# Kernel tuning notes

Hardware: AMD Instinct MI355X
Metric: run time of the kernel (lower is better)

The kernel has to match this reference:

```python
import jax, jax.numpy as jnp
import numpy as np


def setup_inputs() -> dict:
    key = jax.random.key(0)
    ks = jax.random.split(key, 13)
    B, D, H, O = 4096, 2048, 3, 1  # batch, input_dim, hidden layer count, output_dim
    f32 = jnp.float32
    scale = 1.0 / np.sqrt(D)
    return {
        "x": jax.random.normal(ks[0], (B, D), f32),
        "w_mu_h": jax.random.normal(ks[1], (H, D, D), f32) * scale,
        "w_rho_h": jax.random.normal(ks[2], (H, D, D), f32) - 5.0,  # softplus(-5) ~ small std
        "b_mu_h": jax.random.normal(ks[3], (H, D), f32) * scale,
        "b_rho_h": jax.random.normal(ks[4], (H, D), f32) - 5.0,
        "w_mu_o": jax.random.normal(ks[5], (O, D), f32) * scale,
        "w_rho_o": jax.random.normal(ks[6], (O, D), f32) - 5.0,
        "b_mu_o": jax.random.normal(ks[7], (O,), f32) * scale,
        "b_rho_o": jax.random.normal(ks[8], (O,), f32) - 5.0,
        # reparameterization noise (torch.randn_like), passed explicitly for determinism
        "eps_w_h": jax.random.normal(ks[9], (H, D, D), f32),
        "eps_b_h": jax.random.normal(ks[10], (H, D), f32),
        "eps_w_o": jax.random.normal(ks[11], (O, D), f32),
        "eps_b_o": jax.random.normal(ks[12], (O,), f32),
    }


def _vlinear(x, w_mu, w_rho, b_mu, b_rho, eps_w, eps_b):
    # weight = mu + eps * softplus(rho); F.linear(x, W, b) = x @ W.T + b
    w = w_mu + eps_w * jax.nn.softplus(w_rho)
    b = b_mu + eps_b * jax.nn.softplus(b_rho)
    return x @ w.T + b


def reference(x, w_mu_h, w_rho_h, b_mu_h, b_rho_h,
              w_mu_o, w_rho_o, b_mu_o, b_rho_o,
              eps_w_h, eps_b_h, eps_w_o, eps_b_o):
    def step(h, p):
        wm, wr, bm, br, ew, eb = p
        h = jax.nn.relu(_vlinear(h, wm, wr, bm, br, ew, eb))
        return h, None

    h, _ = jax.lax.scan(step, x, (w_mu_h, w_rho_h, b_mu_h, b_rho_h, eps_w_h, eps_b_h))
    return _vlinear(h, w_mu_o, w_rho_o, b_mu_o, b_rho_o, eps_w_o, eps_b_o)
```

## Files before the change

kernel.cpp:

```cpp
#include <hip/hip_runtime.h>

#define BB 4096
#define DD 2048

typedef float f32x4 __attribute__((ext_vector_type(4)));
typedef __bf16 bf16x8 __attribute__((ext_vector_type(8)));

typedef __attribute__((address_space(1))) unsigned int gl_u32;
typedef __attribute__((address_space(3))) unsigned int lds_u32;

#define GLOAD_LDS16(gptr, sptr) \
  __builtin_amdgcn_global_load_lds((gl_u32*)(void*)(gptr), (lds_u32*)(sptr), 16, 0, 0)

__device__ __forceinline__ unsigned short f2bf(float f) {
  unsigned int u = __float_as_uint(f);
  u += 0x7fffu + ((u >> 16) & 1u);
  return (unsigned short)(u >> 16);
}

__device__ __forceinline__ float sp(float x) {
  float t = __expf(-fabsf(x));
  return fmaxf(x, 0.0f) + __logf(1.0f + t);
}

__device__ __forceinline__ void prep_w_vec4(
    const float* __restrict__ mu, const float* __restrict__ rho,
    const float* __restrict__ eps, unsigned short* __restrict__ Wh,
    long long i)
{
  float4 m = ((const float4*)mu)[i];
  float4 r = ((const float4*)rho)[i];
  float4 e = ((const float4*)eps)[i];
  ushort4 o;
  o.x = f2bf(m.x + e.x * sp(r.x));
  o.y = f2bf(m.y + e.y * sp(r.y));
  o.z = f2bf(m.z + e.z * sp(r.z));
  o.w = f2bf(m.w + e.w * sp(r.w));
  ((ushort4*)Wh)[i] = o;
}

__device__ __forceinline__ void prep_f32_vec4(
    const float* __restrict__ mu, const float* __restrict__ rho,
    const float* __restrict__ eps, float* __restrict__ out, long long i)
{
  float4 m = ((const float4*)mu)[i];
  float4 r = ((const float4*)rho)[i];
  float4 e = ((const float4*)eps)[i];
  float4 o;
  o.x = m.x + e.x * sp(r.x);
  o.y = m.y + e.y * sp(r.y);
  o.z = m.z + e.z * sp(r.z);
  o.w = m.w + e.w * sp(r.w);
  ((float4*)out)[i] = o;
}

__global__ __launch_bounds__(512) void prep0_kernel(
    const float* __restrict__ x,
    const float* __restrict__ wmuh, const float* __restrict__ wrhoh,
    const float* __restrict__ bmuh, const float* __restrict__ brhoh,
    const float* __restrict__ epswh, const float* __restrict__ epsbh,
    unsigned short* __restrict__ Wh, unsigned short* __restrict__ Xb,
    float* __restrict__ bh)
{
  const int b = blockIdx.x;
  const int t = threadIdx.x;
  if (b < 512) {
    long long base = (long long)b * 2048 + t;
    #pragma unroll
    for (int j = 0; j < 4; ++j)
      prep_w_vec4(wmuh, wrhoh, epswh, Wh, base + j * 512);
    return;
  }
  if (b < 1536) {
    long long base = (long long)(b - 512) * 2048 + t;
    #pragma unroll
    for (int j = 0; j < 4; ++j) {
      float4 v = ((const float4*)x)[base + j * 512];
      ushort4 o;
      o.x = f2bf(v.x); o.y = f2bf(v.y); o.z = f2bf(v.z); o.w = f2bf(v.w);
      ((ushort4*)Xb)[base + j * 512] = o;
    }
    return;
  }
  prep_f32_vec4(bmuh, brhoh, epsbh, bh, t);
}

#define NGEMM 512

__global__ __launch_bounds__(512, 4) void gemm_relu_fused_kernel(
    const unsigned short* __restrict__ A,
    const unsigned short* __restrict__ W,
    const float* __restrict__ bias,
    unsigned short* __restrict__ C,
    int N, int K, int fuse_prep,
    const float* __restrict__ wmuh, const float* __restrict__ wrhoh,
    const float* __restrict__ bmuh, const float* __restrict__ brhoh,
    const float* __restrict__ wmuo, const float* __restrict__ wrhoo,
    const float* __restrict__ bmuo, const float* __restrict__ brhoo,
    const float* __restrict__ epswh, const float* __restrict__ epsbh,
    const float* __restrict__ epswo, const float* __restrict__ epsbo,
    unsigned short* __restrict__ Wh, float* __restrict__ bh,
    float* __restrict__ wo, float* __restrict__ bo)
{
  __shared__ unsigned short sA[128 * 64];
  __shared__ unsigned short sB[128 * 64];

  const int id = blockIdx.x;
  const int t = threadIdx.x;

  if (id >= NGEMM) {
    const int pb = id - NGEMM;
    if (pb < 1024) {
      long long base = 1048576LL + (long long)pb * 2048 + t;
      #pragma unroll
      for (int j = 0; j < 4; ++j)
        prep_w_vec4(wmuh, wrhoh, epswh, Wh, base + j * 512);
      return;
    }
    #pragma unroll
    for (int j = 0; j < 2; ++j)
      prep_f32_vec4(bmuh, brhoh, epsbh, bh, 512 + j * 512 + t);
    prep_f32_vec4(wmuo, wrhoo, epswo, wo, t);
    if (t == 0) bo[0] = bmuo[0] + epsbo[0] * sp(brhoo[0]);
    return;
  }

  const int w = t >> 6;
  const int l = t & 63;
  const int lq = l >> 4;
  const int lr = l & 15;

  const int p = id & 7;
  const int i4 = id >> 3;
  const int mt = (p & 3) * 8 + (i4 & 7);
  const int nt = (p >> 2) * 8 + (i4 >> 3);
  const int m0 = mt * 128;
  const int n0 = nt * 128;

  const int mw = (w >> 2) * 64;
  const int nw = (w & 3) * 32;

  f32x4 acc[4][2] = {};

  int srow[2], sgc[2];
  #pragma unroll
  for (int i = 0; i < 2; ++i) {
    int c = i * 512 + t;
    srow[i] = c >> 3;
    sgc[i] = (c & 7) ^ (srow[i] & 7);
  }

  for (int kt = 0; kt < K; kt += 64) {
    #pragma unroll
    for (int i = 0; i < 2; ++i) {
      int c = i * 512 + t;
      const unsigned short* ga = A + (size_t)(m0 + srow[i]) * K + kt + sgc[i] * 8;
      GLOAD_LDS16(ga, &sA[c * 8]);
      const unsigned short* gb = W + (size_t)(n0 + srow[i]) * K + kt + sgc[i] * 8;
      GLOAD_LDS16(gb, &sB[c * 8]);
    }
    __syncthreads();

    #pragma unroll
    for (int s = 0; s < 2; ++s) {
      bf16x8 af[4], bfr[2];
      int g = s * 4 + lq;
      #pragma unroll
      for (int i = 0; i < 4; ++i) {
        int ra = mw + i * 16 + lr;
        af[i] = *(const bf16x8*)&sA[ra * 64 + (g ^ (ra & 7)) * 8];
      }
      #pragma unroll
      for (int j = 0; j < 2; ++j) {
        int rb = nw + j * 16 + lr;
        bfr[j] = *(const bf16x8*)&sB[rb * 64 + (g ^ (rb & 7)) * 8];
      }
      #pragma unroll
      for (int i = 0; i < 4; ++i)
        #pragma unroll
        for (int j = 0; j < 2; ++j)
          acc[i][j] = __builtin_amdgcn_mfma_f32_16x16x32_bf16(af[i], bfr[j], acc[i][j], 0, 0, 0);
    }
    __syncthreads();
  }

  #pragma unroll
  for (int j = 0; j < 2; ++j) {
    int n = n0 + nw + j * 16 + lr;
    float bv = bias[n];
    #pragma unroll
    for (int i = 0; i < 4; ++i) {
      int mbase = m0 + mw + i * 16 + lq * 4;
      #pragma unroll
      for (int r = 0; r < 4; ++r) {
        float v = acc[i][j][r] + bv;
        v = fmaxf(v, 0.0f);
        C[(size_t)(mbase + r) * N + n] = f2bf(v);
      }
    }
  }
}

__global__ __launch_bounds__(512, 4) void gemm_relu_kernel(
    const unsigned short* __restrict__ A,
    const unsigned short* __restrict__ W,
    const float* __restrict__ bias,
    unsigned short* __restrict__ C,
    int N, int K)
{
  __shared__ unsigned short sA[128 * 64];
  __shared__ unsigned short sB[128 * 64];

  const int t = threadIdx.x;
  const int w = t >> 6;
  const int l = t & 63;
  const int lq = l >> 4;
  const int lr = l & 15;

  const int id = blockIdx.x;
  const int p = id & 7;
  const int i4 = id >> 3;
  const int mt = (p & 3) * 8 + (i4 & 7);
  const int nt = (p >> 2) * 8 + (i4 >> 3);
  const int m0 = mt * 128;
  const int n0 = nt * 128;

  const int mw = (w >> 2) * 64;
  const int nw = (w & 3) * 32;

  f32x4 acc[4][2] = {};

  int srow[2], sgc[2];
  #pragma unroll
  for (int i = 0; i < 2; ++i) {
    int c = i * 512 + t;
    srow[i] = c >> 3;
    sgc[i] = (c & 7) ^ (srow[i] & 7);
  }

  for (int kt = 0; kt < K; kt += 64) {
    #pragma unroll
    for (int i = 0; i < 2; ++i) {
      int c = i * 512 + t;
      const unsigned short* ga = A + (size_t)(m0 + srow[i]) * K + kt + sgc[i] * 8;
      GLOAD_LDS16(ga, &sA[c * 8]);
      const unsigned short* gb = W + (size_t)(n0 + srow[i]) * K + kt + sgc[i] * 8;
      GLOAD_LDS16(gb, &sB[c * 8]);
    }
    __syncthreads();

    #pragma unroll
    for (int s = 0; s < 2; ++s) {
      bf16x8 af[4], bfr[2];
      int g = s * 4 + lq;
      #pragma unroll
      for (int i = 0; i < 4; ++i) {
        int ra = mw + i * 16 + lr;
        af[i] = *(const bf16x8*)&sA[ra * 64 + (g ^ (ra & 7)) * 8];
      }
      #pragma unroll
      for (int j = 0; j < 2; ++j) {
        int rb = nw + j * 16 + lr;
        bfr[j] = *(const bf16x8*)&sB[rb * 64 + (g ^ (rb & 7)) * 8];
      }
      #pragma unroll
      for (int i = 0; i < 4; ++i)
        #pragma unroll
        for (int j = 0; j < 2; ++j)
          acc[i][j] = __builtin_amdgcn_mfma_f32_16x16x32_bf16(af[i], bfr[j], acc[i][j], 0, 0, 0);
    }
    __syncthreads();
  }

  #pragma unroll
  for (int j = 0; j < 2; ++j) {
    int n = n0 + nw + j * 16 + lr;
    float bv = bias[n];
    #pragma unroll
    for (int i = 0; i < 4; ++i) {
      int mbase = m0 + mw + i * 16 + lq * 4;
      #pragma unroll
      for (int r = 0; r < 4; ++r) {
        float v = acc[i][j][r] + bv;
        v = fmaxf(v, 0.0f);
        C[(size_t)(mbase + r) * N + n] = f2bf(v);
      }
    }
  }
}

__global__ void final_kernel(const unsigned short* __restrict__ H,
                             const float* __restrict__ wo,
                             const float* __restrict__ bo,
                             float* __restrict__ out)
{
  const int row = blockIdx.x * 4 + (threadIdx.x >> 6);
  const int l = threadIdx.x & 63;
  const unsigned short* hr = H + (size_t)row * DD;
  float sum = 0.0f;
  #pragma unroll
  for (int s = 0; s < 4; ++s) {
    int k = s * 512 + l * 8;
    uint4 hv = *(const uint4*)&hr[k];
    float4 w0 = *(const float4*)&wo[k];
    float4 w1 = *(const float4*)&wo[k + 4];
    sum += __uint_as_float(hv.x << 16) * w0.x;
    sum += __uint_as_float(hv.x & 0xffff0000u) * w0.y;
    sum += __uint_as_float(hv.y << 16) * w0.z;
    sum += __uint_as_float(hv.y & 0xffff0000u) * w0.w;
    sum += __uint_as_float(hv.z << 16) * w1.x;
    sum += __uint_as_float(hv.z & 0xffff0000u) * w1.y;
    sum += __uint_as_float(hv.w << 16) * w1.z;
    sum += __uint_as_float(hv.w & 0xffff0000u) * w1.w;
  }
  #pragma unroll
  for (int off = 32; off > 0; off >>= 1)
    sum += __shfl_down(sum, off, 64);
  if (l == 0) out[row] = sum + bo[0];
}

extern "C" void kernel_launch(void* const* d_in, const int* in_sizes, int n_in,
                              void* d_out, int out_size, void* d_ws, size_t ws_size,
                              hipStream_t stream) {
  const float* x     = (const float*)d_in[0];
  const float* wmuh  = (const float*)d_in[1];
  const float* wrhoh = (const float*)d_in[2];
  const float* bmuh  = (const float*)d_in[3];
  const float* brhoh = (const float*)d_in[4];
  const float* wmuo  = (const float*)d_in[5];
  const float* wrhoo = (const float*)d_in[6];
  const float* bmuo  = (const float*)d_in[7];
  const float* brhoo = (const float*)d_in[8];
  const float* epswh = (const float*)d_in[9];
  const float* epsbh = (const float*)d_in[10];
  const float* epswo = (const float*)d_in[11];
  const float* epsbo = (const float*)d_in[12];

  char* ws = (char*)d_ws;
  unsigned short* Wh = (unsigned short*)(ws);
  unsigned short* Xb = (unsigned short*)(ws + 25165824);
  unsigned short* Ha = (unsigned short*)(ws + 25165824 + 16777216);
  unsigned short* Hb = (unsigned short*)(ws + 25165824 + 2 * 16777216);
  float* bh = (float*)(ws + 25165824 + 3 * 16777216);
  float* wo = (float*)(ws + 25165824 + 3 * 16777216 + 24576);
  float* bo = (float*)(ws + 25165824 + 3 * 16777216 + 24576 + 8192);

  prep0_kernel<<<1537, 512, 0, stream>>>(
      x, wmuh, wrhoh, bmuh, brhoh, epswh, epsbh, Wh, Xb, bh);

  gemm_relu_fused_kernel<<<NGEMM + 1025, 512, 0, stream>>>(
      Xb, Wh, bh, Ha, DD, DD, 1,
      wmuh, wrhoh, bmuh, brhoh, wmuo, wrhoo, bmuo, brhoo,
      epswh, epsbh, epswo, epsbo, Wh, bh, wo, bo);

  gemm_relu_kernel<<<NGEMM, 512, 0, stream>>>(Ha, Wh + 1 * 4194304, bh + DD,     Hb, DD, DD);
  gemm_relu_kernel<<<NGEMM, 512, 0, stream>>>(Hb, Wh + 2 * 4194304, bh + 2 * DD, Xb, DD, DD);

  final_kernel<<<BB / 4, 256, 0, stream>>>(Xb, wo, bo, (float*)d_out);
}
```

Before: 304.8 us.

## Fuse output-layer dot product into last hidden GEMM epilogue

The third hidden GEMM no longer writes its bf16 activation matrix. Its epilogue applies bias and ReLU, multiplies by the output weights, and reduces across lanes and waves into per-N-tile partial sums. A small kernel then adds the 16 partials and the output bias. This removes a 16MB store and reload plus the separate output-layer kernel, at the cost of shuffle and LDS reduction work in the epilogue and one extra launch. The shared GEMM code is also factored into inline helpers.

```diff
diff --git a/kernel.cpp b/kernel.cpp
--- a/kernel.cpp
+++ b/kernel.cpp
@@ -87,20 +87,109 @@
 
 #define NGEMM 512
 
+struct GemmCoords { int m0, n0, mw, nw; int srow[2], sgc[2]; };
+
+__device__ __forceinline__ GemmCoords gemm_coords(int id, int t) {
+  GemmCoords g;
+  const int w = t >> 6;
+  const int p = id & 7;
+  const int i4 = id >> 3;
+  const int mt = (p & 3) * 8 + (i4 & 7);
+  const int nt = (p >> 2) * 8 + (i4 >> 3);
+  g.m0 = mt * 128;
+  g.n0 = nt * 128;
+  g.mw = (w >> 2) * 64;
+  g.nw = (w & 3) * 32;
+  #pragma unroll
+  for (int i = 0; i < 2; ++i) {
+    int c = i * 512 + t;
+    g.srow[i] = c >> 3;
+    g.sgc[i] = (c & 7) ^ (g.srow[i] & 7);
+  }
+  return g;
+}
+
+__device__ __forceinline__ void gemm_mainloop(
+    const unsigned short* __restrict__ A,
+    const unsigned short* __restrict__ W,
+    unsigned short* sA, unsigned short* sB,
+    const GemmCoords& gc, int t, f32x4 (&acc)[4][2])
+{
+  const int K = DD;
+  const int l = t & 63;
+  const int lq = l >> 4;
+  const int lr = l & 15;
+  for (int kt = 0; kt < K; kt += 64) {
+    #pragma unroll
+    for (int i = 0; i < 2; ++i) {
+      int c = i * 512 + t;
+      const unsigned short* ga = A + (size_t)(gc.m0 + gc.srow[i]) * K + kt + gc.sgc[i] * 8;
+      GLOAD_LDS16(ga, &sA[c * 8]);
+      const unsigned short* gb = W + (size_t)(gc.n0 + gc.srow[i]) * K + kt + gc.sgc[i] * 8;
+      GLOAD_LDS16(gb, &sB[c * 8]);
+    }
+    __syncthreads();
+
+    #pragma unroll
+    for (int s = 0; s < 2; ++s) {
+      bf16x8 af[4], bfr[2];
+      int g = s * 4 + lq;
+      #pragma unroll
+      for (int i = 0; i < 4; ++i) {
+        int ra = gc.mw + i * 16 + lr;
+        af[i] = *(const bf16x8*)&sA[ra * 64 + (g ^ (ra & 7)) * 8];
+      }
+      #pragma unroll
+      for (int j = 0; j < 2; ++j) {
+        int rb = gc.nw + j * 16 + lr;
+        bfr[j] = *(const bf16x8*)&sB[rb * 64 + (g ^ (rb & 7)) * 8];
+      }
+      #pragma unroll
+      for (int i = 0; i < 4; ++i)
+        #pragma unroll
+        for (int j = 0; j < 2; ++j)
+          acc[i][j] = __builtin_amdgcn_mfma_f32_16x16x32_bf16(af[i], bfr[j], acc[i][j], 0, 0, 0);
+    }
+    __syncthreads();
+  }
+}
+
+__device__ __forceinline__ void gemm_epilogue_store(
+    const GemmCoords& gc, int t, f32x4 (&acc)[4][2],
+    const float* __restrict__ bias, unsigned short* __restrict__ C)
+{
+  const int N = DD;
+  const int l = t & 63;
+  const int lq = l >> 4;
+  const int lr = l & 15;
+  #pragma unroll
+  for (int j = 0; j < 2; ++j) {
+    int n = gc.n0 + gc.nw + j * 16 + lr;
+    float bv = bias[n];
+    #pragma unroll
+    for (int i = 0; i < 4; ++i) {
+      int mbase = gc.m0 + gc.mw + i * 16 + lq * 4;
+      #pragma unroll
+      for (int r = 0; r < 4; ++r) {
+        float v = fmaxf(acc[i][j][r] + bv, 0.0f);
+        C[(size_t)(mbase + r) * N + n] = f2bf(v);
+      }
+    }
+  }
+}
+
 __global__ __launch_bounds__(512, 4) void gemm_relu_fused_kernel(
     const unsigned short* __restrict__ A,
     const unsigned short* __restrict__ W,
     const float* __restrict__ bias,
     unsigned short* __restrict__ C,
-    int N, int K, int fuse_prep,
     const float* __restrict__ wmuh, const float* __restrict__ wrhoh,
     const float* __restrict__ bmuh, const float* __restrict__ brhoh,
     const float* __restrict__ wmuo, const float* __restrict__ wrhoo,
-    const float* __restrict__ bmuo, const float* __restrict__ brhoo,
     const float* __restrict__ epswh, const float* __restrict__ epsbh,
-    const float* __restrict__ epswo, const float* __restrict__ epsbo,
+    const float* __restrict__ epswo,
     unsigned short* __restrict__ Wh, float* __restrict__ bh,
-    float* __restrict__ wo, float* __restrict__ bo)
+    float* __restrict__ wo)
 {
   __shared__ unsigned short sA[128 * 64];
   __shared__ unsigned short sB[128 * 64];
@@ -121,202 +210,104 @@
     for (int j = 0; j < 2; ++j)
       prep_f32_vec4(bmuh, brhoh, epsbh, bh, 512 + j * 512 + t);
     prep_f32_vec4(wmuo, wrhoo, epswo, wo, t);
-    if (t == 0) bo[0] = bmuo[0] + epsbo[0] * sp(brhoo[0]);
     return;
   }
 
-  const int w = t >> 6;
-  const int l = t & 63;
-  const int lq = l >> 4;
-  const int lr = l & 15;
-
-  const int p = id & 7;
-  const int i4 = id >> 3;
-  const int mt = (p & 3) * 8 + (i4 & 7);
-  const int nt = (p >> 2) * 8 + (i4 >> 3);
-  const int m0 = mt * 128;
-  const int n0 = nt * 128;
-
-  const int mw = (w >> 2) * 64;
-  const int nw = (w & 3) * 32;
-
+  GemmCoords gc = gemm_coords(id, t);
   f32x4 acc[4][2] = {};
-
-  int srow[2], sgc[2];
-  #pragma unroll
-  for (int i = 0; i < 2; ++i) {
-    int c = i * 512 + t;
-    srow[i] = c >> 3;
-    sgc[i] = (c & 7) ^ (srow[i] & 7);
-  }
-
-  for (int kt = 0; kt < K; kt += 64) {
-    #pragma unroll
-    for (int i = 0; i < 2; ++i) {
-      int c = i * 512 + t;
-      const unsigned short* ga = A + (size_t)(m0 + srow[i]) * K + kt + sgc[i] * 8;
-      GLOAD_LDS16(ga, &sA[c * 8]);
-      const unsigned short* gb = W + (size_t)(n0 + srow[i]) * K + kt + sgc[i] * 8;
-      GLOAD_LDS16(gb, &sB[c * 8]);
-    }
-    __syncthreads();
-
-    #pragma unroll
-    for (int s = 0; s < 2; ++s) {
-      bf16x8 af[4], bfr[2];
-      int g = s * 4 + lq;
-      #pragma unroll
-      for (int i = 0; i < 4; ++i) {
-        int ra = mw + i * 16 + lr;
-        af[i] = *(const bf16x8*)&sA[ra * 64 + (g ^ (ra & 7)) * 8];
-      }
-      #pragma unroll
-      for (int j = 0; j < 2; ++j) {
-        int rb = nw + j * 16 + lr;
-        bfr[j] = *(const bf16x8*)&sB[rb * 64 + (g ^ (rb & 7)) * 8];
-      }
-      #pragma unroll
-      for (int i = 0; i < 4; ++i)
-        #pragma unroll
-        for (int j = 0; j < 2; ++j)
-          acc[i][j] = __builtin_amdgcn_mfma_f32_16x16x32_bf16(af[i], bfr[j], acc[i][j], 0, 0, 0);
-    }
-    __syncthreads();
-  }
-
-  #pragma unroll
-  for (int j = 0; j < 2; ++j) {
-    int n = n0 + nw + j * 16 + lr;
-    float bv = bias[n];
-    #pragma unroll
-    for (int i = 0; i < 4; ++i) {
-      int mbase = m0 + mw + i * 16 + lq * 4;
-      #pragma unroll
-      for (int r = 0; r < 4; ++r) {
-        float v = acc[i][j][r] + bv;
-        v = fmaxf(v, 0.0f);
-        C[(size_t)(mbase + r) * N + n] = f2bf(v);
-      }
-    }
-  }
+  gemm_mainloop(A, W, sA, sB, gc, t, acc);
+  gemm_epilogue_store(gc, t, acc, bias, C);
 }
 
 __global__ __launch_bounds__(512, 4) void gemm_relu_kernel(
     const unsigned short* __restrict__ A,
     const unsigned short* __restrict__ W,
     const float* __restrict__ bias,
-    unsigned short* __restrict__ C,
-    int N, int K)
+    unsigned short* __restrict__ C)
 {
   __shared__ unsigned short sA[128 * 64];
   __shared__ unsigned short sB[128 * 64];
-
   const int t = threadIdx.x;
+  GemmCoords gc = gemm_coords(blockIdx.x, t);
+  f32x4 acc[4][2] = {};
+  gemm_mainloop(A, W, sA, sB, gc, t, acc);
+  gemm_epilogue_store(gc, t, acc, bias, C);
+}
+
+__global__ __launch_bounds__(512, 4) void gemm_relu_dot_kernel(
+    const unsigned short* __restrict__ A,
+    const unsigned short* __restrict__ W,
+    const float* __restrict__ bias,
+    const float* __restrict__ wo,
+    float* __restrict__ Pbuf)
+{
+  __shared__ unsigned short sA[128 * 64];
+  __shared__ unsigned short sB[128 * 64];
+  const int t = threadIdx.x;
+
+  GemmCoords gc = gemm_coords(blockIdx.x, t);
+  f32x4 acc[4][2] = {};
+  gemm_mainloop(A, W, sA, sB, gc, t, acc);
+
+  const int l = t & 63;
   const int w = t >> 6;
-  const int l = t & 63;
   const int lq = l >> 4;
   const int lr = l & 15;
-
-  const int id = blockIdx.x;
-  const int p = id & 7;
-  const int i4 = id >> 3;
-  const int mt = (p & 3) * 8 + (i4 & 7);
-  const int nt = (p >> 2) * 8 + (i4 >> 3);
-  const int m0 = mt * 128;
-  const int n0 = nt * 128;
-
-  const int mw = (w >> 2) * 64;
-  const int nw = (w & 3) * 32;
-
-  f32x4 acc[4][2] = {};
-
-  int srow[2], sgc[2];
-  #pragma unroll
-  for (int i = 0; i < 2; ++i) {
-    int c = i * 512 + t;
-    srow[i] = c >> 3;
-    sgc[i] = (c & 7) ^ (srow[i] & 7);
-  }
-
-  for (int kt = 0; kt < K; kt += 64) {
-    #pragma unroll
-    for (int i = 0; i < 2; ++i) {
-      int c = i * 512 + t;
-      const unsigned short* ga = A + (size_t)(m0 + srow[i]) * K + kt + sgc[i] * 8;
-      GLOAD_LDS16(ga, &sA[c * 8]);
-      const unsigned short* gb = W + (size_t)(n0 + srow[i]) * K + kt + sgc[i] * 8;
-      GLOAD_LDS16(gb, &sB[c * 8]);
-    }
-    __syncthreads();
-
-    #pragma unroll
-    for (int s = 0; s < 2; ++s) {
-      bf16x8 af[4], bfr[2];
-      int g = s * 4 + lq;
-      #pragma unroll
-      for (int i = 0; i < 4; ++i) {
-        int ra = mw + i * 16 + lr;
-        af[i] = *(const bf16x8*)&sA[ra * 64 + (g ^ (ra & 7)) * 8];
+  const int nq = w & 3;
+
+  float bv[2], wv[2];
+  #pragma unroll
+  for (int j = 0; j < 2; ++j) {
+    int n = gc.n0 + gc.nw + j * 16 + lr;
+    bv[j] = bias[n];
+    wv[j] = wo[n];
+  }
+  float partial[4][4];
+  #pragma unroll
+  for (int i = 0; i < 4; ++i)
+    #pragma unroll
+    for (int r = 0; r < 4; ++r)
+      partial[i][r] = fmaxf(acc[i][0][r] + bv[0], 0.0f) * wv[0]
+                    + fmaxf(acc[i][1][r] + bv[1], 0.0f) * wv[1];
+
+  #pragma unroll
+  for (int d = 1; d <= 8; d <<= 1)
+    #pragma unroll
+    for (int i = 0; i < 4; ++i)
+      #pragma unroll
+      for (int r = 0; r < 4; ++r)
+        partial[i][r] += __shfl_xor(partial[i][r], d, 64);
+
+  float* sRed = (float*)sA;
+  if (lr == 0) {
+    #pragma unroll
+    for (int i = 0; i < 4; ++i)
+      #pragma unroll
+      for (int r = 0; r < 4; ++r) {
+        int row = gc.mw + i * 16 + lq * 4 + r;
+        sRed[row * 4 + nq] = partial[i][r];
       }
-      #pragma unroll
-      for (int j = 0; j < 2; ++j) {
-        int rb = nw + j * 16 + lr;
-        bfr[j] = *(const bf16x8*)&sB[rb * 64 + (g ^ (rb & 7)) * 8];
-      }
-      #pragma unroll
-      for (int i = 0; i < 4; ++i)
-        #pragma unroll
-        for (int j = 0; j < 2; ++j)
-          acc[i][j] = __builtin_amdgcn_mfma_f32_16x16x32_bf16(af[i], bfr[j], acc[i][j], 0, 0, 0);
-    }
-    __syncthreads();
-  }
-
-  #pragma unroll
-  for (int j = 0; j < 2; ++j) {
-    int n = n0 + nw + j * 16 + lr;
-    float bv = bias[n];
-    #pragma unroll
-    for (int i = 0; i < 4; ++i) {
-      int mbase = m0 + mw + i * 16 + lq * 4;
-      #pragma unroll
-      for (int r = 0; r < 4; ++r) {
-        float v = acc[i][j][r] + bv;
-        v = fmaxf(v, 0.0f);
-        C[(size_t)(mbase + r) * N + n] = f2bf(v);
-      }
-    }
-  }
-}
-
-__global__ void final_kernel(const unsigned short* __restrict__ H,
-                             const float* __restrict__ wo,
-                             const float* __restrict__ bo,
-                             float* __restrict__ out)
-{
-  const int row = blockIdx.x * 4 + (threadIdx.x >> 6);
-  const int l = threadIdx.x & 63;
-  const unsigned short* hr = H + (size_t)row * DD;
-  float sum = 0.0f;
-  #pragma unroll
-  for (int s = 0; s < 4; ++s) {
-    int k = s * 512 + l * 8;
-    uint4 hv = *(const uint4*)&hr[k];
-    float4 w0 = *(const float4*)&wo[k];
-    float4 w1 = *(const float4*)&wo[k + 4];
-    sum += __uint_as_float(hv.x << 16) * w0.x;
-    sum += __uint_as_float(hv.x & 0xffff0000u) * w0.y;
-    sum += __uint_as_float(hv.y << 16) * w0.z;
-    sum += __uint_as_float(hv.y & 0xffff0000u) * w0.w;
-    sum += __uint_as_float(hv.z << 16) * w1.x;
-    sum += __uint_as_float(hv.z & 0xffff0000u) * w1.y;
-    sum += __uint_as_float(hv.w << 16) * w1.z;
-    sum += __uint_as_float(hv.w & 0xffff0000u) * w1.w;
-  }
-  #pragma unroll
-  for (int off = 32; off > 0; off >>= 1)
-    sum += __shfl_down(sum, off, 64);
-  if (l == 0) out[row] = sum + bo[0];
+  }
+  __syncthreads();
+  if (t < 128) {
+    float s = sRed[t * 4 + 0] + sRed[t * 4 + 1] + sRed[t * 4 + 2] + sRed[t * 4 + 3];
+    int nt = gc.n0 >> 7;
+    Pbuf[nt * BB + gc.m0 + t] = s;
+  }
+}
+
+__global__ __launch_bounds__(256) void reduce_out_kernel(
+    const float* __restrict__ Pbuf,
+    const float* __restrict__ bmuo, const float* __restrict__ brhoo,
+    const float* __restrict__ epsbo,
+    float* __restrict__ out)
+{
+  const int m = blockIdx.x * 256 + threadIdx.x;
+  float s = bmuo[0] + epsbo[0] * sp(brhoo[0]);
+  #pragma unroll
+  for (int nt = 0; nt < 16; ++nt)
+    s += Pbuf[nt * BB + m];
+  out[m] = s;
 }
 
 extern "C" void kernel_launch(void* const* d_in, const int* in_sizes, int n_in,
@@ -341,20 +332,23 @@
   unsigned short* Xb = (unsigned short*)(ws + 25165824);
   unsigned short* Ha = (unsigned short*)(ws + 25165824 + 16777216);
   unsigned short* Hb = (unsigned short*)(ws + 25165824 + 2 * 16777216);
-  float* bh = (float*)(ws + 25165824 + 3 * 16777216);
-  float* wo = (float*)(ws + 25165824 + 3 * 16777216 + 24576);
-  float* bo = (float*)(ws + 25165824 + 3 * 16777216 + 24576 + 8192);
+  float* bh   = (float*)(ws + 25165824 + 3 * 16777216);
+  float* wo   = (float*)(ws + 25165824 + 3 * 16777216 + 24576);
+  float* Pbuf = (float*)(ws + 25165824 + 3 * 16777216 + 24576 + 8192);
 
   prep0_kernel<<<1537, 512, 0, stream>>>(
       x, wmuh, wrhoh, bmuh, brhoh, epswh, epsbh, Wh, Xb, bh);
 
   gemm_relu_fused_kernel<<<NGEMM + 1025, 512, 0, stream>>>(
-      Xb, Wh, bh, Ha, DD, DD, 1,
-      wmuh, wrhoh, bmuh, brhoh, wmuo, wrhoo, bmuo, brhoo,
-      epswh, epsbh, epswo, epsbo, Wh, bh, wo, bo);
-
-  gemm_relu_kernel<<<NGEMM, 512, 0, stream>>>(Ha, Wh + 1 * 4194304, bh + DD,     Hb, DD, DD);
-  gemm_relu_kernel<<<NGEMM, 512, 0, stream>>>(Hb, Wh + 2 * 4194304, bh + 2 * DD, Xb, DD, DD);
-
-  final_kernel<<<BB / 4, 256, 0, stream>>>(Xb, wo, bo, (float*)d_out);
-}
+      Xb, Wh, bh, Ha,
+      wmuh, wrhoh, bmuh, brhoh, wmuo, wrhoo,
+      epswh, epsbh, epswo, Wh, bh, wo);
+
+  gemm_relu_kernel<<<NGEMM, 512, 0, stream>>>(Ha, Wh + 1 * 4194304, bh + DD, Hb);
+
+  gemm_relu_dot_kernel<<<NGEMM, 512, 0, stream>>>(
+      Hb, Wh + 2 * 4194304, bh + 2 * DD, wo, Pbuf);
+
+  reduce_out_kernel<<<BB / 256, 256, 0, stream>>>(
+      Pbuf, bmuo, brhoo, epsbo, (float*)d_out);
+}
```

After: 298.3 us. 2.1% less time.
